# Performance work log

Hardware: AMD Instinct MI355X
Metric: run time of the kernel (lower is better)

The kernel has to match this reference:

```python
import jax, jax.numpy as jnp
import numpy as np

QB = 127.0      # 2**(bits_act-1) - 1 for bits_act=8
EPS = 1e-5

def act_quant_ste(x):
    # per-tensor int8 absmax quantization (per_token_act=False), straight-through
    scale = QB / jnp.maximum(jnp.max(jnp.abs(x)), EPS)
    q = jnp.clip(jnp.round(x * scale), -QB, QB) / scale
    return x + jax.lax.stop_gradient(q - x)

def weight_quant_ste(w):
    # BitNet b1.58 ternary quantization: scale = mean(|W|)
    beta = jnp.maximum(jnp.mean(jnp.abs(w)), EPS)
    q = jnp.clip(jnp.round(w / beta), -1.0, 1.0) * beta
    return w + jax.lax.stop_gradient(q - w)

def layernorm(x, w, b):
    mu = jnp.mean(x, axis=-1, keepdims=True)
    var = jnp.mean(jnp.square(x - mu), axis=-1, keepdims=True)
    return (x - mu) * jax.lax.rsqrt(var + EPS) * w + b

def bitlinear(x, w):
    return jnp.einsum('bsd,fd->bsf', act_quant_ste(x), weight_quant_ste(w))

def setup_inputs() -> dict:
    key = jax.random.key(0)
    k1, k2, k3 = jax.random.split(key, 3)
    d_model, d_ff = 2048, 8192
    B, S = 4, 2048
    x = jax.random.normal(k1, (B, S, d_model), dtype=jnp.float32)
    ln_w = jnp.ones((d_model,), dtype=jnp.float32)
    ln_b = jnp.zeros((d_model,), dtype=jnp.float32)
    w1 = jax.random.normal(k2, (d_ff, d_model), dtype=jnp.float32) * (1.0 / np.sqrt(d_model))
    w2 = jax.random.normal(k3, (d_model, d_ff), dtype=jnp.float32) * (1.0 / np.sqrt(d_ff))
    return {"x": x, "ln_w": ln_w, "ln_b": ln_b, "w1": w1, "w2": w2}

def reference(x, ln_w, ln_b, w1, w2):
    x_ln = layernorm(x, ln_w, ln_b)             # Sub-LN before quantized linear
    h = jax.nn.gelu(bitlinear(x_ln, w1), approximate=False)  # F.gelu default = exact
    y = bitlinear(h, w2)
    return y
```

## Files before the change

### kernel.cpp

```cpp
#include <hip/hip_runtime.h>

typedef signed char char8v __attribute__((ext_vector_type(8)));
typedef signed char char4v __attribute__((ext_vector_type(4)));
typedef short short8 __attribute__((ext_vector_type(8)));
typedef int int32x4 __attribute__((ext_vector_type(4)));

static constexpr int DM = 2048;
static constexpr int DF = 8192;
static constexpr int MT = 8192;
static constexpr int CH = 4096;
static constexpr double INVND = 1.0 / 16777216.0;

static constexpr size_t OFF_STATS = 256;
static constexpr size_t OFF_QX   = OFF_STATS + 65536;
static constexpr size_t OFF_QW1  = OFF_QX  + (size_t)MT * DM;
static constexpr size_t OFF_QW2  = OFF_QW1 + (size_t)DF * DM;
static constexpr size_t OFF_HACC = OFF_QW2 + (size_t)DM * DF;

__device__ __forceinline__ float waveSum(float v) {
#pragma unroll
  for (int o = 32; o > 0; o >>= 1) v += __shfl_xor(v, o, 64);
  return v;
}
__device__ __forceinline__ double waveSumD(double v) {
#pragma unroll
  for (int o = 32; o > 0; o >>= 1) v += __shfl_xor(v, o, 64);
  return v;
}
__device__ __forceinline__ float waveMax(float v) {
#pragma unroll
  for (int o = 32; o > 0; o >>= 1) v = fmaxf(v, __shfl_xor(v, o, 64));
  return v;
}
__device__ __forceinline__ float gelu_exact(float v) {
  return 0.5f * v * (1.0f + erff(v * 0.70710678118654752f));
}
__device__ __forceinline__ signed char q8(float v, float lo, float hi) {
  return (signed char)fminf(fmaxf(rintf(v), lo), hi);
}

__global__ __launch_bounds__(64) void zero_k(float* p) { p[threadIdx.x] = 0.f; }

__global__ __launch_bounds__(256) void abssum_k(const float4* __restrict__ w, int n4,
                                                double* __restrict__ out) {
  double s = 0.0;
  for (int i = blockIdx.x * 256 + threadIdx.x; i < n4; i += gridDim.x * 256) {
    float4 v = w[i];
    s += (double)fabsf(v.x) + (double)fabsf(v.y) + (double)fabsf(v.z) + (double)fabsf(v.w);
  }
  s = waveSumD(s);
  __shared__ double sm[4];
  if ((threadIdx.x & 63) == 0) sm[threadIdx.x >> 6] = s;
  __syncthreads();
  if (threadIdx.x == 0) atomicAdd(out, sm[0] + sm[1] + sm[2] + sm[3]);
}

__global__ __launch_bounds__(256) void ln_k(const float* __restrict__ x, const float* __restrict__ w,
                                            const float* __restrict__ b, float* __restrict__ stats,
                                            unsigned* __restrict__ amax) {
  __shared__ float sm[4];
  const int row = blockIdx.x, t = threadIdx.x;
  const float4* xr = (const float4*)(x + (size_t)row * DM);
  float4 v0 = xr[t], v1 = xr[t + 256];
  float s = v0.x + v0.y + v0.z + v0.w + v1.x + v1.y + v1.z + v1.w;
  s = waveSum(s);
  if ((t & 63) == 0) sm[t >> 6] = s;
  __syncthreads();
  const float mu = (sm[0] + sm[1] + sm[2] + sm[3]) * (1.0f / DM);
  __syncthreads();
  float d[8] = {v0.x - mu, v0.y - mu, v0.z - mu, v0.w - mu,
                v1.x - mu, v1.y - mu, v1.z - mu, v1.w - mu};
  float sq = 0.f;
#pragma unroll
  for (int i = 0; i < 8; i++) sq += d[i] * d[i];
  sq = waveSum(sq);
  if ((t & 63) == 0) sm[t >> 6] = sq;
  __syncthreads();
  const float var = (sm[0] + sm[1] + sm[2] + sm[3]) * (1.0f / DM);
  const float rstd = 1.0f / sqrtf(var + 1e-5f);
  __syncthreads();
  const float4* wr = (const float4*)w;
  const float4* br = (const float4*)b;
  float4 w0 = wr[t], w1v = wr[t + 256], b0 = br[t], b1v = br[t + 256];
  float m = 0.f;
  m = fmaxf(m, fabsf(d[0] * rstd * w0.x + b0.x));
  m = fmaxf(m, fabsf(d[1] * rstd * w0.y + b0.y));
  m = fmaxf(m, fabsf(d[2] * rstd * w0.z + b0.z));
  m = fmaxf(m, fabsf(d[3] * rstd * w0.w + b0.w));
  m = fmaxf(m, fabsf(d[4] * rstd * w1v.x + b1v.x));
  m = fmaxf(m, fabsf(d[5] * rstd * w1v.y + b1v.y));
  m = fmaxf(m, fabsf(d[6] * rstd * w1v.z + b1v.z));
  m = fmaxf(m, fabsf(d[7] * rstd * w1v.w + b1v.w));
  m = waveMax(m);
  if ((t & 63) == 0) sm[t >> 6] = m;
  __syncthreads();
  if (t == 0) {
    float mm = fmaxf(fmaxf(sm[0], sm[1]), fmaxf(sm[2], sm[3]));
    stats[2 * row] = mu;
    stats[2 * row + 1] = rstd;
    atomicMax(amax, __float_as_uint(mm));
  }
}

__global__ __launch_bounds__(256) void quantx_k(const float* __restrict__ x, const float* __restrict__ w,
                                                const float* __restrict__ b, const float* __restrict__ stats,
                                                const float* __restrict__ fam, signed char* __restrict__ qx) {
  const int row = blockIdx.x, t = threadIdx.x;
  const float mu = stats[2 * row], rstd = stats[2 * row + 1];
  const float sc = 127.0f / fmaxf(fam[0], 1e-5f);
  const float4* xr = (const float4*)(x + (size_t)row * DM);
  const float4* wr = (const float4*)w;
  const float4* br = (const float4*)b;
  float4 v0 = xr[2 * t], v1 = xr[2 * t + 1];
  float4 w0 = wr[2 * t], w1v = wr[2 * t + 1];
  float4 b0 = br[2 * t], b1v = br[2 * t + 1];
  char8v o;
  o[0] = q8(((v0.x - mu) * rstd * w0.x + b0.x) * sc, -127.f, 127.f);
  o[1] = q8(((v0.y - mu) * rstd * w0.y + b0.y) * sc, -127.f, 127.f);
  o[2] = q8(((v0.z - mu) * rstd * w0.z + b0.z) * sc, -127.f, 127.f);
  o[3] = q8(((v0.w - mu) * rstd * w0.w + b0.w) * sc, -127.f, 127.f);
  o[4] = q8(((v1.x - mu) * rstd * w1v.x + b1v.x) * sc, -127.f, 127.f);
  o[5] = q8(((v1.y - mu) * rstd * w1v.y + b1v.y) * sc, -127.f, 127.f);
  o[6] = q8(((v1.z - mu) * rstd * w1v.z + b1v.z) * sc, -127.f, 127.f);
  o[7] = q8(((v1.w - mu) * rstd * w1v.w + b1v.w) * sc, -127.f, 127.f);
  *(char8v*)(qx + (size_t)row * DM + t * 8) = o;
}

__global__ __launch_bounds__(256) void quantw_k(const float4* __restrict__ w,
                                                const double* __restrict__ sumabs,
                                                signed char* __restrict__ qw, int n4) {
  const float beta = fmaxf((float)(sumabs[0] * INVND), 1e-5f);
  const float rb = 1.0f / beta;
  for (int i = blockIdx.x * 256 + threadIdx.x; i < n4; i += gridDim.x * 256) {
    float4 v = w[i];
    char4v o;
    o[0] = q8(v.x * rb, -1.f, 1.f);
    o[1] = q8(v.y * rb, -1.f, 1.f);
    o[2] = q8(v.z * rb, -1.f, 1.f);
    o[3] = q8(v.w * rb, -1.f, 1.f);
    *(char4v*)(qw + (size_t)i * 4) = o;
  }
}

__global__ __launch_bounds__(256) void quanth_k(const short8* __restrict__ hacc,
                                                const double* __restrict__ dsum,
                                                const float* __restrict__ fam,
                                                signed char* __restrict__ qh, int n8) {
  const float beta = fmaxf((float)(dsum[0] * INVND), 1e-5f);
  const float s1 = beta * fmaxf(fam[0], 1e-5f) * (1.0f / 127.0f);
  const float sc2 = 127.0f / fmaxf(fam[1], 1e-5f);
  for (int i = blockIdx.x * 256 + threadIdx.x; i < n8; i += gridDim.x * 256) {
    short8 v = hacc[i];
    char8v o;
#pragma unroll
    for (int j = 0; j < 8; j++) {
      const float g = gelu_exact((float)v[j] * s1);
      o[j] = q8(g * sc2, -127.f, 127.f);
    }
    *(char8v*)(qh + (size_t)i * 8) = o;
  }
}

__device__ __forceinline__ void gll16(const signed char* g, signed char* l) {
  __builtin_amdgcn_global_load_lds((const __attribute__((address_space(1))) void*)g,
                                   (__attribute__((address_space(3))) void*)l, 16, 0, 0);
}

template <int EPI>
__global__ __launch_bounds__(256, 4) void gemm_i8(const signed char* __restrict__ A,
                                                  const signed char* __restrict__ B,
                                                  void* __restrict__ Cv, int M, int N, int K,
                                                  int bandrows,
                                                  const double* __restrict__ p_sumw,
                                                  const float* __restrict__ p_amax,
                                                  unsigned* __restrict__ amax_out) {
  __shared__ signed char As[128 * 64];
  __shared__ signed char Bs[128 * 64];
  const int tid = threadIdx.x;
  const int wid = tid >> 6, lane = tid & 63;

  const int xcd = (int)blockIdx.x & 7;
  const int idx = (int)blockIdx.x >> 3;
  const int by = xcd * bandrows + (idx % bandrows);
  const int bx = idx / bandrows;
  const int m0 = by * 128, n0 = bx * 128;
  const int wm = (wid >> 1) * 64, wn = (wid & 1) * 64;

  int32x4 acc[4][4];
#pragma unroll
  for (int i = 0; i < 4; i++)
#pragma unroll
    for (int j = 0; j < 4; j++) acc[i][j] = int32x4{0, 0, 0, 0};

  const int srow = tid >> 2;
  const int scol = (tid & 3) * 16;
  const signed char* gA = A + (size_t)(m0 + srow) * K + scol;
  const signed char* gB = B + (size_t)(n0 + srow) * K + scol;
  const size_t rowK64 = (size_t)64 * K;

  const int lrow = lane & 15;
  const int lkb = (lane >> 4) * 16;
  const int aoff = (wm + lrow) * 64 + lkb;
  const int boff = (wn + lrow) * 64 + lkb;

  for (int k0 = 0; k0 < K; k0 += 64) {
    __syncthreads();
    gll16(gA + k0,          As + wid * 1024);
    gll16(gA + k0 + rowK64, As + 4096 + wid * 1024);
    gll16(gB + k0,          Bs + wid * 1024);
    gll16(gB + k0 + rowK64, Bs + 4096 + wid * 1024);
    __syncthreads();

    int32x4 af[4], bfv[4];
#pragma unroll
    for (int m = 0; m < 4; m++) af[m] = *(const int32x4*)(As + aoff + m * 1024);
#pragma unroll
    for (int n = 0; n < 4; n++) bfv[n] = *(const int32x4*)(Bs + boff + n * 1024);
#pragma unroll
    for (int m = 0; m < 4; m++)
#pragma unroll
      for (int n = 0; n < 4; n++)
        acc[m][n] = __builtin_amdgcn_mfma_i32_16x16x64_i8(af[m], bfv[n], acc[m][n], 0, 0, 0);
  }

  const float beta = fmaxf((float)(p_sumw[0] * INVND), 1e-5f);
  const float s = beta * fmaxf(p_amax[0], 1e-5f) * (1.0f / 127.0f);
  const int crow0 = m0 + wm + ((lane >> 4) << 2);
  const int ccol0 = n0 + wn + (lane & 15);
  float lmax = 0.f;
#pragma unroll
  for (int m = 0; m < 4; m++) {
#pragma unroll
    for (int n = 0; n < 4; n++) {
#pragma unroll
      for (int j = 0; j < 4; j++) {
        const float a = (float)acc[m][n][j];
        const size_t idx2 = (size_t)(crow0 + m * 16 + j) * N + (ccol0 + n * 16);
        if (EPI == 1) {
          ((short*)Cv)[idx2] = (short)fminf(fmaxf(a, -32767.f), 32767.f);
          lmax = fmaxf(lmax, fabsf(gelu_exact(a * s)));
        } else {
          ((float*)Cv)[idx2] = a * s;
        }
      }
    }
  }
  if (EPI == 1) {
    lmax = waveMax(lmax);
    if (lane == 0) atomicMax(amax_out, __float_as_uint(lmax));
  }
}

extern "C" void kernel_launch(void* const* d_in, const int* in_sizes, int n_in,
                              void* d_out, int out_size, void* d_ws, size_t ws_size,
                              hipStream_t stream) {
  const float* x = (const float*)d_in[0];
  const float* lnw = (const float*)d_in[1];
  const float* lnb = (const float*)d_in[2];
  const float* w1 = (const float*)d_in[3];
  const float* w2 = (const float*)d_in[4];
  float* out = (float*)d_out;

  char* ws = (char*)d_ws;
  double* dsum = (double*)ws;
  float* fam = (float*)(ws + 16);
  float* stats = (float*)(ws + OFF_STATS);
  signed char* qx = (signed char*)(ws + OFF_QX);
  signed char* qw1 = (signed char*)(ws + OFF_QW1);
  signed char* qw2 = (signed char*)(ws + OFF_QW2);
  short* hacc = (short*)(ws + OFF_HACC);
  signed char* qh = (signed char*)(ws + OFF_QX);

  zero_k<<<1, 64, 0, stream>>>((float*)ws);
  abssum_k<<<2048, 256, 0, stream>>>((const float4*)w1, (DF * DM) / 4, &dsum[0]);
  abssum_k<<<2048, 256, 0, stream>>>((const float4*)w2, (DM * DF) / 4, &dsum[1]);
  ln_k<<<MT, 256, 0, stream>>>(x, lnw, lnb, stats, (unsigned*)&fam[0]);
  quantx_k<<<MT, 256, 0, stream>>>(x, lnw, lnb, stats, fam, qx);
  quantw_k<<<2048, 256, 0, stream>>>((const float4*)w1, &dsum[0], qw1, (DF * DM) / 4);
  quantw_k<<<2048, 256, 0, stream>>>((const float4*)w2, &dsum[1], qw2, (DM * DF) / 4);

  gemm_i8<1><<<dim3((DF / 128) * (MT / 128)), 256, 0, stream>>>(qx, qw1, hacc, MT, DF, DM,
                                                                MT / 128 / 8, &dsum[0], &fam[0],
                                                                (unsigned*)&fam[1]);
  for (int c = 0; c < MT / CH; c++) {
    quanth_k<<<2048, 256, 0, stream>>>((const short8*)(hacc + (size_t)c * CH * DF), &dsum[0], fam,
                                       qh, (CH * DF) / 8);
    gemm_i8<0><<<dim3((DM / 128) * (CH / 128)), 256, 0, stream>>>(qh, qw2, out + (size_t)c * CH * DM,
                                                                  CH, DM, DF, CH / 128 / 8,
                                                                  &dsum[1], &fam[1], nullptr);
  }
}
```

Baseline: 966.3 us.

## Double-buffer LDS tiles in int8 GEMM to overlap global loads with MFMA

Replaces the single LDS tile pair with a two-stage buffer. Each iteration issues the async global-to-LDS loads for the next K slice, then waits only for the current slice with a partial vmcnt before running the MFMAs. This hides global memory latency behind compute. The epilogue is also split so the GELU amax pass and the stores run in separate loops. The change doubles LDS use to 32KB per block, which may reduce occupancy at 4 blocks per CU, and it depends on hand-written waitcnt counts being correct.

Result: slower. 1.025 ms (+6.0%).

```diff
diff --git a/kernel.cpp b/kernel.cpp
--- a/kernel.cpp
+++ b/kernel.cpp
@@ -174,8 +174,7 @@
                                                   const double* __restrict__ p_sumw,
                                                   const float* __restrict__ p_amax,
                                                   unsigned* __restrict__ amax_out) {
-  __shared__ signed char As[128 * 64];
-  __shared__ signed char Bs[128 * 64];
+  __shared__ __align__(16) signed char smem[32768];
   const int tid = threadIdx.x;
   const int wid = tid >> 6, lane = tid & 63;
 
@@ -203,51 +202,85 @@
   const int aoff = (wm + lrow) * 64 + lkb;
   const int boff = (wn + lrow) * 64 + lkb;
 
+#define STAGE(buf, k0)                                            \
+  {                                                               \
+    signed char* base_ = smem + ((buf) << 14);                    \
+    gll16(gA + (k0), base_ + wid * 1024);                         \
+    gll16(gA + (k0) + rowK64, base_ + 4096 + wid * 1024);         \
+    gll16(gB + (k0), base_ + 8192 + wid * 1024);                  \
+    gll16(gB + (k0) + rowK64, base_ + 12288 + wid * 1024);        \
+  }
+
+  STAGE(0, 0);
+  int cur = 0;
   for (int k0 = 0; k0 < K; k0 += 64) {
-    __syncthreads();
-    gll16(gA + k0,          As + wid * 1024);
-    gll16(gA + k0 + rowK64, As + 4096 + wid * 1024);
-    gll16(gB + k0,          Bs + wid * 1024);
-    gll16(gB + k0 + rowK64, Bs + 4096 + wid * 1024);
-    __syncthreads();
-
+    if (k0 + 64 < K) {
+      STAGE(cur ^ 1, k0 + 64);
+      asm volatile("s_waitcnt vmcnt(4)" ::: "memory");
+    } else {
+      asm volatile("s_waitcnt vmcnt(0)" ::: "memory");
+    }
+    __builtin_amdgcn_s_barrier();
+    asm volatile("" ::: "memory");
+
+    const signed char* Ab = smem + (cur << 14);
+    const signed char* Bb = Ab + 8192;
     int32x4 af[4], bfv[4];
 #pragma unroll
-    for (int m = 0; m < 4; m++) af[m] = *(const int32x4*)(As + aoff + m * 1024);
-#pragma unroll
-    for (int n = 0; n < 4; n++) bfv[n] = *(const int32x4*)(Bs + boff + n * 1024);
+    for (int m = 0; m < 4; m++) af[m] = *(const int32x4*)(Ab + aoff + m * 1024);
+#pragma unroll
+    for (int n = 0; n < 4; n++) bfv[n] = *(const int32x4*)(Bb + boff + n * 1024);
 #pragma unroll
     for (int m = 0; m < 4; m++)
 #pragma unroll
       for (int n = 0; n < 4; n++)
         acc[m][n] = __builtin_amdgcn_mfma_i32_16x16x64_i8(af[m], bfv[n], acc[m][n], 0, 0, 0);
-  }
+
+    asm volatile("" ::: "memory");
+    __builtin_amdgcn_s_barrier();
+    cur ^= 1;
+  }
+#undef STAGE
 
   const float beta = fmaxf((float)(p_sumw[0] * INVND), 1e-5f);
   const float s = beta * fmaxf(p_amax[0], 1e-5f) * (1.0f / 127.0f);
   const int crow0 = m0 + wm + ((lane >> 4) << 2);
   const int ccol0 = n0 + wn + (lane & 15);
-  float lmax = 0.f;
-#pragma unroll
-  for (int m = 0; m < 4; m++) {
-#pragma unroll
-    for (int n = 0; n < 4; n++) {
+
+  if (EPI == 1) {
+    float lmax = 0.f;
+#pragma unroll
+    for (int m = 0; m < 4; m++)
+#pragma unroll
+      for (int n = 0; n < 4; n++)
+#pragma unroll
+        for (int j = 0; j < 4; j++)
+          lmax = fmaxf(lmax, fabsf(gelu_exact((float)acc[m][n][j] * s)));
+    lmax = waveMax(lmax);
+    if (lane == 0) atomicMax(amax_out, __float_as_uint(lmax));
+#pragma unroll
+    for (int m = 0; m < 4; m++) {
 #pragma unroll
       for (int j = 0; j < 4; j++) {
-        const float a = (float)acc[m][n][j];
-        const size_t idx2 = (size_t)(crow0 + m * 16 + j) * N + (ccol0 + n * 16);
-        if (EPI == 1) {
-          ((short*)Cv)[idx2] = (short)fminf(fmaxf(a, -32767.f), 32767.f);
-          lmax = fmaxf(lmax, fabsf(gelu_exact(a * s)));
-        } else {
-          ((float*)Cv)[idx2] = a * s;
+        const size_t rowb = (size_t)(crow0 + m * 16 + j) * N + ccol0;
+#pragma unroll
+        for (int n = 0; n < 4; n++) {
+          const float a = (float)acc[m][n][j];
+          ((short*)Cv)[rowb + n * 16] = (short)fminf(fmaxf(a, -32767.f), 32767.f);
         }
       }
     }
-  }
-  if (EPI == 1) {
-    lmax = waveMax(lmax);
-    if (lane == 0) atomicMax(amax_out, __float_as_uint(lmax));
+  } else {
+#pragma unroll
+    for (int m = 0; m < 4; m++) {
+#pragma unroll
+      for (int j = 0; j < 4; j++) {
+        const size_t rowb = (size_t)(crow0 + m * 16 + j) * N + ccol0;
+#pragma unroll
+        for (int n = 0; n < 4; n++)
+          ((float*)Cv)[rowb + n * 16] = (float)acc[m][n][j] * s;
+      }
+    }
   }
 }
 
```
